# Kernel optimization log

Measured on AMD Instinct MI355X. Metric: run time of the kernel, lower is better.

Reference implementation:

```python
import jax, jax.numpy as jnp
import numpy as np

B, C, HH, WW, QK = 8, 64, 64, 64, 8


def setup_inputs() -> dict:
    key = jax.random.key(0)
    ks = jax.random.split(key, 22)
    s = 0.05
    def W(k, o, i):
        return jax.random.normal(k, (o, i), jnp.float32) * s
    def bvec(k, o):
        return jax.random.normal(k, (o,), jnp.float32) * s
    return {
        "H_in": jax.random.normal(ks[0], (B, C, HH, WW), jnp.float32),
        "M_prev": jax.random.normal(ks[1], (B, C, HH, WW), jnp.float32),
        "wq": W(ks[2], QK, C), "bq": bvec(ks[3], QK),
        "wkh": W(ks[4], QK, C), "bkh": bvec(ks[5], QK),
        "wvh": W(ks[6], C, C), "bvh": bvec(ks[7], C),
        "wkm": W(ks[8], QK, C), "bkm": bvec(ks[9], QK),
        "wvm": W(ks[10], C, C), "bvm": bvec(ks[11], C),
        "wz": W(ks[12], C, 2 * C), "bz": bvec(ks[13], C),
        "wo": W(ks[14], C, 2 * C), "bo": bvec(ks[15], C),
        "wg": W(ks[16], C, 2 * C), "bg": bvec(ks[17], C),
        "wi": W(ks[18], C, 2 * C), "bi": bvec(ks[19], C),
    }


def _conv1x1(w, b, x):
    # x: [B, Cin, N] -> [B, Cout, N]
    return jnp.einsum("oc,bcn->bon", w, x) + b[None, :, None]


def reference(H_in, M_prev, wq, bq, wkh, bkh, wvh, bvh, wkm, bkm, wvm, bvm,
              wz, bz, wo, bo, wg, bg, wi, bi):
    Bn, Cn, Hn, Wn = H_in.shape
    N = Hn * Wn
    h = H_in.reshape(Bn, Cn, N)   # flatten spatial
    m = M_prev.reshape(Bn, Cn, N)

    Q = _conv1x1(wq, bq, h)       # [B, QK, N]
    Kh = _conv1x1(wkh, bkh, h)
    Vh = _conv1x1(wvh, bvh, h)    # [B, C, N]
    Km = _conv1x1(wkm, bkm, m)
    Vm = _conv1x1(wvm, bvm, m)

    scale = jnp.asarray(np.sqrt(Q.shape[1]), Q.dtype)
    # scores: [B, N, N], softmax over last axis
    Ah = jax.nn.softmax(jnp.einsum("bcn,bcm->bnm", Q, Kh) / scale, axis=-1)
    Am = jax.nn.softmax(jnp.einsum("bcn,bcm->bnm", Q, Km) / scale, axis=-1)
    # Zh = Vh @ Ah^T : [B, C, N]
    Zh = jnp.einsum("bcm,bnm->bcn", Vh, Ah)
    Zm = jnp.einsum("bcm,bnm->bcn", Vm, Am)

    Z = _conv1x1(wz, bz, jnp.concatenate([Zh, Zm], axis=1))  # [B, C, N]
    concat = jnp.concatenate([h, Z], axis=1)                  # [B, 2C, N]
    O_t = jax.nn.sigmoid(_conv1x1(wo, bo, concat))
    G_t = jnp.tanh(_conv1x1(wg, bg, concat))
    I_t = jax.nn.sigmoid(_conv1x1(wi, bi, concat))

    M_t = (1.0 - I_t) * m + I_t * G_t
    H_out = O_t * M_t
    return (H_out.reshape(Bn, Cn, Hn, Wn), M_t.reshape(Bn, Cn, Hn, Wn))
```

## Files before the change

### kernel.cpp

```cpp
#include <hip/hip_runtime.h>

#define BATCH 8
#define CC 64
#define NN 4096
#define SCL 0.51006973f

typedef __attribute__((ext_vector_type(8))) short s16x8;
typedef __attribute__((ext_vector_type(4))) short s16x4;
typedef __attribute__((ext_vector_type(4))) float f32x4;
typedef __attribute__((ext_vector_type(2))) unsigned int uint2v;

__device__ __forceinline__ short f2bf(float f) {
  unsigned u = __builtin_bit_cast(unsigned, f);
  u += 0x7fffu + ((u >> 16) & 1u);
  return (short)(u >> 16);
}
__device__ __forceinline__ float bf2f(short h) {
  unsigned u = ((unsigned)(unsigned short)h) << 16;
  return __builtin_bit_cast(float, u);
}
__device__ __forceinline__ unsigned cvt_pk_bf16(float lo, float hi) {
  unsigned r;
  asm volatile("v_cvt_pk_bf16_f32 %0, %1, %2" : "=v"(r) : "v"(lo), "v"(hi));
  return r;
}

__device__ __forceinline__ int kperm(int kk) {
  int hh = (kk >> 5) & 1, g = (kk >> 3) & 3, c = kk & 7;
  return hh * 32 + (c < 4 ? (g << 2) + c : 16 + ((g ^ 2) << 2) + (c - 4));
}

__global__ void prep_weights_kernel(const float* __restrict__ wz, const float* __restrict__ bz,
                                    const float* __restrict__ wo, const float* __restrict__ bo,
                                    const float* __restrict__ wg, const float* __restrict__ bg,
                                    const float* __restrict__ wi, const float* __restrict__ bi,
                                    const float* __restrict__ wq, const float* __restrict__ bq,
                                    const float* __restrict__ wkh, const float* __restrict__ bkh,
                                    const float* __restrict__ wvh, const float* __restrict__ bvh,
                                    const float* __restrict__ wkm, const float* __restrict__ bkm,
                                    const float* __restrict__ wvm, const float* __restrict__ bvm,
                                    short* __restrict__ Weff, float* __restrict__ beff,
                                    short* __restrict__ Wcat, float* __restrict__ bias) {
  int i = blockIdx.x * 256 + threadIdx.x;
  const float* wjs[3] = {wo, wg, wi};
  const float* bjs[3] = {bo, bg, bi};
  const float gsc[3] = {1.44269504f, 2.88539008f, 1.44269504f};
  if (i < 36864) {
    int j = i / 12288, rem = i % 12288, o = rem / 192, k = rem % 192;
    const float* wj = wjs[j];
    float v;
    if (k < 64) {
      v = wj[o * 128 + k];
    } else {
      v = 0.f;
      #pragma unroll 8
      for (int t = 0; t < 64; ++t) v += wj[o * 128 + 64 + t] * wz[t * 128 + (k - 64)];
    }
    Weff[i] = f2bf(v * gsc[j]);
  } else if (i < 37056) {
    int i2 = i - 36864;
    int j = i2 >> 6, o = i2 & 63;
    const float* wj = wjs[j];
    float v = bjs[j][o];
    #pragma unroll 8
    for (int t = 0; t < 64; ++t) v += wj[o * 128 + 64 + t] * bz[t];
    beff[i2] = v * gsc[j];
  } else if (i < 47296) {
    int i2 = i - 37056;
    int src = i2 / 5120, rem = i2 % 5120, row = rem >> 6, col = rem & 63;
    float v;
    if (src == 0) {
      if (row < 64) v = wvh[row * 64 + col];
      else if (row < 72) v = wq[(row - 64) * 64 + col] * SCL;
      else v = wkh[(row - 72) * 64 + col];
    } else {
      if (row < 64) v = wvm[row * 64 + col];
      else if (row < 72) v = wkm[(row - 64) * 64 + col];
      else v = 0.f;
    }
    Wcat[i2] = f2bf(v);
  } else if (i < 47456) {
    int i3 = i - 47296;
    int src = i3 / 80, row = i3 % 80;
    float v;
    if (src == 0) v = (row < 64) ? bvh[row] : (row < 72 ? bq[row - 64] * SCL : bkh[row - 72]);
    else          v = (row < 64) ? bvm[row] : (row < 72 ? bkm[row - 64] : 0.f);
    bias[i3] = v;
  }
}

__global__ __launch_bounds__(256) void proj_kernel(
    const float* __restrict__ H_in, const float* __restrict__ M_prev,
    const short* __restrict__ Wcat, const float* __restrict__ bias,
    short* __restrict__ Qt, short* __restrict__ Kht, short* __restrict__ Kmt,
    short* __restrict__ Vh, short* __restrict__ Vm) {
  int src = blockIdx.x & 1;
  int n0 = ((blockIdx.x >> 1) & 63) << 6;
  int b = blockIdx.x >> 7;
  int tid = threadIdx.x, w = tid >> 6, l = tid & 63, lg = l >> 4, ll = l & 15;

  const float* __restrict__ X = src ? M_prev : H_in;
  short* __restrict__ Vp = src ? Vm : Vh;

  __shared__ __align__(16) short Xt[64][68];
  __shared__ __align__(16) short Ot[64][76];

  {
    int c = tid & 63, q = tid >> 6;
    const float* xs = X + ((size_t)((b << 6) + c)) * NN + n0 + q * 16;
    #pragma unroll
    for (int j = 0; j < 4; ++j) {
      float4 v = *(const float4*)(xs + j * 4);
      Xt[q * 16 + j * 4 + 0][c] = f2bf(v.x);
      Xt[q * 16 + j * 4 + 1][c] = f2bf(v.y);
      Xt[q * 16 + j * 4 + 2][c] = f2bf(v.z);
      Xt[q * 16 + j * 4 + 3][c] = f2bf(v.w);
    }
  }
  __syncthreads();

  f32x4 acc[5];
  #pragma unroll
  for (int ot = 0; ot < 5; ++ot)
    #pragma unroll
    for (int r = 0; r < 4; ++r) acc[ot][r] = bias[src * 80 + ot * 16 + lg * 4 + r];

  #pragma unroll
  for (int kk = 0; kk < 2; ++kk) {
    s16x8 bx = *(const s16x8*)&Xt[w * 16 + ll][kk * 32 + lg * 8];
    #pragma unroll
    for (int ot = 0; ot < 5; ++ot) {
      s16x8 aw = *(const s16x8*)(Wcat + ((size_t)(src * 80 + ot * 16 + ll)) * 64 + kk * 32 + lg * 8);
      acc[ot] = __builtin_amdgcn_mfma_f32_16x16x32_bf16(aw, bx, acc[ot], 0, 0, 0);
    }
  }

  #pragma unroll
  for (int ot = 0; ot < 4; ++ot)
    #pragma unroll
    for (int r = 0; r < 4; ++r)
      Ot[ot * 16 + lg * 4 + r][w * 16 + ll] = f2bf(acc[ot][r]);

  {
    int n = n0 + w * 16 + ll;
    int pr = (n & ~63) + kperm(n & 63);
    #pragma unroll
    for (int r = 0; r < 4; ++r) {
      float v = acc[4][r];
      if (src == 0) {
        if (lg < 2) Qt[((size_t)(b * NN + n)) * 8 + (lg * 4 + r)] = f2bf(v);
        else        Kht[((size_t)(b * NN + pr)) * 8 + ((lg - 2) * 4 + r)] = f2bf(v);
      } else {
        if (lg < 2) Kmt[((size_t)(b * NN + pr)) * 8 + (lg * 4 + r)] = f2bf(v);
      }
    }
  }
  __syncthreads();

  #pragma unroll
  for (int h = 0; h < 2; ++h) {
    int ci = tid + h * 256;
    int row = ci >> 3, seg = ci & 7;
    *(s16x8*)(Vp + ((size_t)((b << 6) + row)) * NN + n0 + seg * 8) =
        *(const s16x8*)&Ot[row][seg * 8];
  }
}

__global__ __launch_bounds__(256, 8) void attn_kernel(
    const short* __restrict__ Qt, const short* __restrict__ Kht, const short* __restrict__ Kmt,
    const short* __restrict__ Vh, const short* __restrict__ Vm,
    short* __restrict__ Zp, float* __restrict__ dnb) {
  unsigned vb = (blockIdx.x & 7) * 256 + (blockIdx.x >> 3);
  int kh = vb >> 10;
  int b  = (vb >> 7) & 7;
  int s  = (vb >> 6) & 1;
  int q0 = (vb & 63) << 6;
  int tid = threadIdx.x;
  int w = tid >> 6, l = tid & 63, lg = l >> 4, ll = l & 15;
  const bool lo32 = (l < 32);

  const short* __restrict__ Kp = s ? Kmt : Kht;
  const short* __restrict__ Vp = s ? Vm : Vh;

  __shared__ __align__(16) short Vt[2][64][64];
  __shared__ __align__(16) short Ktl[2][64][8];
  short* VtF = &Vt[0][0][0];
  short* KtF = &Ktl[0][0][0];

  s16x8 bq = {};
  if (lg == 0) bq = *(const s16x8*)(Qt + ((size_t)(b * NN + q0 + w * 16 + ll)) * 8);
  s16x8 ones;
  #pragma unroll
  for (int i = 0; i < 8; ++i) ones[i] = (short)0x3F80;

  f32x4 accZ[4];
  f32x4 accDn = {0.f, 0.f, 0.f, 0.f};
  #pragma unroll
  for (int cs = 0; cs < 4; ++cs) accZ[cs] = (f32x4){0.f, 0.f, 0.f, 0.f};

  const int vOff0 = ll * 64 + ((lg ^ (ll & 7)) << 3);
  const int vOff1 = ll * 64 + (((lg ^ 4) ^ (ll & 7)) << 3);
  const int kOff  = ll * 8;

  const int row0 = w * 8 + (l >> 3);
  const int swz  = ((l & 7) ^ (l >> 3)) << 3;
  const short* vsrc0 = Vp + ((size_t)((b << 6) + row0)) * NN + kh * 2048 + swz;
  const short* vsrc1 = Vp + ((size_t)((b << 6) + 32 + row0)) * NN + kh * 2048 + swz;
  const short* ksrc  = Kp + ((size_t)(b * NN) + kh * 2048 + l) * 8;

#define GLDS(src_, dst_) \
  __builtin_amdgcn_global_load_lds((const __attribute__((address_space(1))) void*)(src_), \
                                   (__attribute__((address_space(3))) void*)(dst_), 16, 0, 0)
#define STAGE(bufL, ktL) do { \
    GLDS(vsrc0 + (ktL) * 64, VtF + (bufL) * 4096 + w * 512); \
    GLDS(vsrc1 + (ktL) * 64, VtF + (bufL) * 4096 + 2048 + w * 512); \
    if (w == 0) GLDS(ksrc + (ktL) * 512, KtF + (bufL) * 512); \
  } while (0)

  auto compute = [&](int bufL) {
    float p[4][4];
    #pragma unroll
    for (int hh = 0; hh < 2; ++hh) {
      #pragma unroll
      for (int par = 0; par < 2; ++par) {
        s16x8 ak = *(const s16x8*)(KtF + bufL * 512 + (hh * 32 + par * 16) * 8 + kOff);
        f32x4 sc = __builtin_amdgcn_mfma_f32_16x16x32_bf16(ak, bq, (f32x4){0.f,0.f,0.f,0.f}, 0, 0, 0);
        #pragma unroll
        for (int r = 0; r < 4; ++r) p[hh * 2 + par][r] = __builtin_amdgcn_exp2f(sc[r]);
      }
    }
    unsigned wkv[4][2];
    #pragma unroll
    for (int ks = 0; ks < 4; ++ks) {
      wkv[ks][0] = cvt_pk_bf16(p[ks][0], p[ks][1]);
      wkv[ks][1] = cvt_pk_bf16(p[ks][2], p[ks][3]);
    }
    #pragma unroll
    for (int hh = 0; hh < 2; ++hh) {
      unsigned o0 = wkv[hh * 2 + 1][0], o1 = wkv[hh * 2 + 1][1];
      uint2v pr0 = __builtin_amdgcn_permlane32_swap(o0, o0, false, false);
      uint2v pr1 = __builtin_amdgcn_permlane32_swap(o1, o1, false, false);
      unsigned sw0 = lo32 ? pr0.y : pr0.x;
      unsigned sw1 = lo32 ? pr1.y : pr1.x;
      union { unsigned u[4]; s16x8 v; } bpu;
      bpu.u[0] = wkv[hh * 2][0];
      bpu.u[1] = wkv[hh * 2][1];
      bpu.u[2] = sw0;
      bpu.u[3] = sw1;
      s16x8 bp = bpu.v;
      accDn = __builtin_amdgcn_mfma_f32_16x16x32_bf16(ones, bp, accDn, 0, 0, 0);
      const int vo = hh ? vOff1 : vOff0;
      #pragma unroll
      for (int cs = 0; cs < 4; ++cs) {
        s16x8 av = *(const s16x8*)(VtF + bufL * 4096 + cs * 1024 + vo);
        accZ[cs] = __builtin_amdgcn_mfma_f32_16x16x32_bf16(av, bp, accZ[cs], 0, 0, 0);
      }
    }
  };

  STAGE(0, 0);
  #pragma unroll 1
  for (int kt2 = 0; kt2 < 16; ++kt2) {
    int kt = kt2 * 2;
    asm volatile("s_waitcnt vmcnt(0)" ::: "memory");
    __builtin_amdgcn_s_barrier();
    STAGE(1, kt + 1);
    compute(0);
    asm volatile("s_waitcnt vmcnt(0)" ::: "memory");
    __builtin_amdgcn_s_barrier();
    if (kt2 < 15) STAGE(0, kt + 2);
    compute(1);
  }

  #pragma unroll
  for (int cs = 0; cs < 4; ++cs) {
    s16x4 o4;
    #pragma unroll
    for (int r = 0; r < 4; ++r) o4[r] = f2bf(accZ[cs][r]);
    *(s16x4*)(Zp + ((size_t)((kh * 8 + b) * NN + q0 + w * 16 + ll)) * 128 + s * 64 + cs * 16 + lg * 4) = o4;
  }
  if (l < 16)
    dnb[((size_t)(kh * 16 + b * 2 + s)) * NN + q0 + w * 16 + l] = accDn[0];
#undef STAGE
#undef GLDS
}

__global__ __launch_bounds__(256) void gates_kernel(
    const float* __restrict__ H_in, const float* __restrict__ M_prev,
    const short* __restrict__ Zp, const float* __restrict__ dnb,
    const short* __restrict__ Weff, const float* __restrict__ beff,
    float* __restrict__ out) {
  int b = blockIdx.x >> 7;
  int n0 = (blockIdx.x & 127) << 5;
  int tid = threadIdx.x, w = tid >> 6, l = tid & 63, lg = l >> 4, ll = l & 15;
  __shared__ __align__(16) short Xt[32][200];

  {
    int c = tid & 63, q = tid >> 6;
    const float* xs = H_in + ((size_t)((b << 6) + c)) * NN + n0 + q * 8;
    #pragma unroll
    for (int j = 0; j < 2; ++j) {
      float4 v = *(const float4*)(xs + j * 4);
      Xt[q * 8 + j * 4 + 0][c] = f2bf(v.x);
      Xt[q * 8 + j * 4 + 1][c] = f2bf(v.y);
      Xt[q * 8 + j * 4 + 2][c] = f2bf(v.z);
      Xt[q * 8 + j * 4 + 3][c] = f2bf(v.w);
    }
  }
  {
    int n = tid >> 3, cq = tid & 7, sidx = cq >> 2;
    const short* z0 = Zp + ((size_t)(b * NN + n0 + n)) * 128 + cq * 16;
    const short* z1 = Zp + ((size_t)((8 + b) * NN + n0 + n)) * 128 + cq * 16;
    float d0 = dnb[((size_t)(b * 2 + sidx)) * NN + n0 + n];
    float d1 = dnb[((size_t)(16 + b * 2 + sidx)) * NN + n0 + n];
    float rd = __builtin_amdgcn_rcpf(d0 + d1);
    s16x8 a0 = *(const s16x8*)z0;
    s16x8 a1 = *(const s16x8*)z1;
    s16x8 b0 = *(const s16x8*)(z0 + 8);
    s16x8 b1 = *(const s16x8*)(z1 + 8);
    s16x8 o0, o1;
    #pragma unroll
    for (int j = 0; j < 8; ++j) {
      o0[j] = f2bf((bf2f(a0[j]) + bf2f(a1[j])) * rd);
      o1[j] = f2bf((bf2f(b0[j]) + bf2f(b1[j])) * rd);
    }
    *(s16x8*)&Xt[n][64 + cq * 16] = o0;
    *(s16x8*)&Xt[n][64 + cq * 16 + 8] = o1;
  }
  __syncthreads();

  f32x4 acc[3][2];
  #pragma unroll
  for (int j = 0; j < 3; ++j)
    #pragma unroll
    for (int ns = 0; ns < 2; ++ns)
      #pragma unroll
      for (int r = 0; r < 4; ++r) acc[j][ns][r] = beff[j * 64 + w * 16 + lg * 4 + r];

  #pragma unroll
  for (int kk = 0; kk < 6; ++kk) {
    s16x8 aw[3];
    #pragma unroll
    for (int j = 0; j < 3; ++j)
      aw[j] = *(const s16x8*)(Weff + ((size_t)(j * 64 + w * 16 + ll)) * 192 + kk * 32 + lg * 8);
    #pragma unroll
    for (int ns = 0; ns < 2; ++ns) {
      s16x8 bx = *(const s16x8*)&Xt[ns * 16 + ll][kk * 32 + lg * 8];
      #pragma unroll
      for (int j = 0; j < 3; ++j)
        acc[j][ns] = __builtin_amdgcn_mfma_f32_16x16x32_bf16(aw[j], bx, acc[j][ns], 0, 0, 0);
    }
  }

  float* Hout = out;
  float* Mout = out + (size_t)BATCH * CC * NN;
  #pragma unroll
  for (int ns = 0; ns < 2; ++ns) {
    #pragma unroll
    for (int r = 0; r < 4; ++r) {
      int c = w * 16 + lg * 4 + r;
      int n = n0 + ns * 16 + ll;
      size_t idx = ((size_t)((b << 6) + c)) * NN + n;
      float xo = acc[0][ns][r], xg = acc[1][ns][r], xi = acc[2][ns][r];
      float o  = __builtin_amdgcn_rcpf(1.f + __builtin_amdgcn_exp2f(-xo));
      float g  = 2.f * __builtin_amdgcn_rcpf(1.f + __builtin_amdgcn_exp2f(-xg)) - 1.f;
      float ii = __builtin_amdgcn_rcpf(1.f + __builtin_amdgcn_exp2f(-xi));
      float m  = M_prev[idx];
      float mt = (1.f - ii) * m + ii * g;
      Mout[idx] = mt;
      Hout[idx] = o * mt;
    }
  }
}

extern "C" void kernel_launch(void* const* d_in, const int* in_sizes, int n_in,
                              void* d_out, int out_size, void* d_ws, size_t ws_size,
                              hipStream_t stream) {
  (void)in_sizes; (void)n_in; (void)out_size; (void)ws_size;
  const float* H_in  = (const float*)d_in[0];
  const float* M_prev= (const float*)d_in[1];
  const float* wq  = (const float*)d_in[2];
  const float* bq  = (const float*)d_in[3];
  const float* wkh = (const float*)d_in[4];
  const float* bkh = (const float*)d_in[5];
  const float* wvh = (const float*)d_in[6];
  const float* bvh = (const float*)d_in[7];
  const float* wkm = (const float*)d_in[8];
  const float* bkm = (const float*)d_in[9];
  const float* wvm = (const float*)d_in[10];
  const float* bvm = (const float*)d_in[11];
  const float* wz  = (const float*)d_in[12];
  const float* bz  = (const float*)d_in[13];
  const float* wo  = (const float*)d_in[14];
  const float* bo  = (const float*)d_in[15];
  const float* wg  = (const float*)d_in[16];
  const float* bg  = (const float*)d_in[17];
  const float* wi  = (const float*)d_in[18];
  const float* bi  = (const float*)d_in[19];

  char* ws = (char*)d_ws;
  size_t off = 0;
  auto alloc = [&](size_t bytes) -> void* {
    void* p = ws + off;
    off += (bytes + 255) & ~(size_t)255;
    return p;
  };
  short* Weff = (short*)alloc(3 * 64 * 192 * 2);
  float* beff = (float*)alloc(192 * 4);
  short* Wcat = (short*)alloc(2 * 80 * 64 * 2);
  float* bias = (float*)alloc(160 * 4);
  short* Qt   = (short*)alloc((size_t)BATCH * NN * 8 * 2);
  short* Kht  = (short*)alloc((size_t)BATCH * NN * 8 * 2);
  short* Kmt  = (short*)alloc((size_t)BATCH * NN * 8 * 2);
  short* Vh   = (short*)alloc((size_t)BATCH * CC * NN * 2);
  short* Vm   = (short*)alloc((size_t)BATCH * CC * NN * 2);
  short* Zp   = (short*)alloc((size_t)2 * BATCH * NN * 128 * 2);
  float* dnb  = (float*)alloc((size_t)2 * BATCH * 2 * NN * 4);

  prep_weights_kernel<<<186, 256, 0, stream>>>(wz, bz, wo, bo, wg, bg, wi, bi,
                                               wq, bq, wkh, bkh, wvh, bvh, wkm, bkm, wvm, bvm,
                                               Weff, beff, Wcat, bias);
  proj_kernel<<<1024, 256, 0, stream>>>(H_in, M_prev, Wcat, bias, Qt, Kht, Kmt, Vh, Vm);
  attn_kernel<<<2048, 256, 0, stream>>>(Qt, Kht, Kmt, Vh, Vm, Zp, dnb);
  gates_kernel<<<1024, 256, 0, stream>>>(H_in, M_prev, Zp, dnb, Weff, beff, (float*)d_out);
}
```

Before: 191.4 us.

## Process two query tiles per wave in attention to reuse K/V LDS loads

Each attention block now covers 128 queries instead of 64. Each wave computes two 16-query sub-tiles, so every K and V fragment read from LDS feeds two MFMAs, and the grid is halved. This cuts LDS traffic and global K/V staging per query. It also wraps the MFMA section in s_setprio to favour matrix issue. The cost is roughly doubled accumulator registers, with occupancy lowered to 4 blocks, and fewer blocks to hide load latency.

```diff
diff --git a/kernel.cpp b/kernel.cpp
--- a/kernel.cpp
+++ b/kernel.cpp
@@ -166,15 +166,16 @@
   }
 }
 
-__global__ __launch_bounds__(256, 8) void attn_kernel(
+__global__ __launch_bounds__(256, 4) void attn_kernel(
     const short* __restrict__ Qt, const short* __restrict__ Kht, const short* __restrict__ Kmt,
     const short* __restrict__ Vh, const short* __restrict__ Vm,
     short* __restrict__ Zp, float* __restrict__ dnb) {
-  unsigned vb = (blockIdx.x & 7) * 256 + (blockIdx.x >> 3);
-  int kh = vb >> 10;
-  int b  = (vb >> 7) & 7;
-  int s  = (vb >> 6) & 1;
-  int q0 = (vb & 63) << 6;
+  unsigned vb = (blockIdx.x & 7) * 128 + (blockIdx.x >> 3);
+  int qt = vb & 31;
+  int s  = (vb >> 5) & 1;
+  int b  = (vb >> 6) & 7;
+  int kh = (vb >> 9) & 1;
+  int q0 = qt << 7;
   int tid = threadIdx.x;
   int w = tid >> 6, l = tid & 63, lg = l >> 4, ll = l & 15;
   const bool lo32 = (l < 32);
@@ -187,16 +188,20 @@
   short* VtF = &Vt[0][0][0];
   short* KtF = &Ktl[0][0][0];
 
-  s16x8 bq = {};
-  if (lg == 0) bq = *(const s16x8*)(Qt + ((size_t)(b * NN + q0 + w * 16 + ll)) * 8);
+  s16x8 bqA = {}, bqB = {};
+  if (lg == 0) {
+    bqA = *(const s16x8*)(Qt + ((size_t)(b * NN + q0 + w * 32 + ll)) * 8);
+    bqB = *(const s16x8*)(Qt + ((size_t)(b * NN + q0 + w * 32 + 16 + ll)) * 8);
+  }
   s16x8 ones;
   #pragma unroll
   for (int i = 0; i < 8; ++i) ones[i] = (short)0x3F80;
-
-  f32x4 accZ[4];
-  f32x4 accDn = {0.f, 0.f, 0.f, 0.f};
-  #pragma unroll
-  for (int cs = 0; cs < 4; ++cs) accZ[cs] = (f32x4){0.f, 0.f, 0.f, 0.f};
+  const f32x4 fz = {0.f, 0.f, 0.f, 0.f};
+
+  f32x4 accZA[4], accZB[4];
+  f32x4 accDnA = fz, accDnB = fz;
+  #pragma unroll
+  for (int cs = 0; cs < 4; ++cs) { accZA[cs] = fz; accZB[cs] = fz; }
 
   const int vOff0 = ll * 64 + ((lg ^ (ll & 7)) << 3);
   const int vOff1 = ll * 64 + (((lg ^ 4) ^ (ll & 7)) << 3);
@@ -218,43 +223,51 @@
   } while (0)
 
   auto compute = [&](int bufL) {
-    float p[4][4];
     #pragma unroll
     for (int hh = 0; hh < 2; ++hh) {
+      float pA[2][4], pB[2][4];
       #pragma unroll
       for (int par = 0; par < 2; ++par) {
         s16x8 ak = *(const s16x8*)(KtF + bufL * 512 + (hh * 32 + par * 16) * 8 + kOff);
-        f32x4 sc = __builtin_amdgcn_mfma_f32_16x16x32_bf16(ak, bq, (f32x4){0.f,0.f,0.f,0.f}, 0, 0, 0);
+        f32x4 scA = __builtin_amdgcn_mfma_f32_16x16x32_bf16(ak, bqA, fz, 0, 0, 0);
+        f32x4 scB = __builtin_amdgcn_mfma_f32_16x16x32_bf16(ak, bqB, fz, 0, 0, 0);
         #pragma unroll
-        for (int r = 0; r < 4; ++r) p[hh * 2 + par][r] = __builtin_amdgcn_exp2f(sc[r]);
+        for (int r = 0; r < 4; ++r) {
+          pA[par][r] = __builtin_amdgcn_exp2f(scA[r]);
+          pB[par][r] = __builtin_amdgcn_exp2f(scB[r]);
+        }
       }
-    }
-    unsigned wkv[4][2];
-    #pragma unroll
-    for (int ks = 0; ks < 4; ++ks) {
-      wkv[ks][0] = cvt_pk_bf16(p[ks][0], p[ks][1]);
-      wkv[ks][1] = cvt_pk_bf16(p[ks][2], p[ks][3]);
-    }
-    #pragma unroll
-    for (int hh = 0; hh < 2; ++hh) {
-      unsigned o0 = wkv[hh * 2 + 1][0], o1 = wkv[hh * 2 + 1][1];
-      uint2v pr0 = __builtin_amdgcn_permlane32_swap(o0, o0, false, false);
-      uint2v pr1 = __builtin_amdgcn_permlane32_swap(o1, o1, false, false);
-      unsigned sw0 = lo32 ? pr0.y : pr0.x;
-      unsigned sw1 = lo32 ? pr1.y : pr1.x;
-      union { unsigned u[4]; s16x8 v; } bpu;
-      bpu.u[0] = wkv[hh * 2][0];
-      bpu.u[1] = wkv[hh * 2][1];
-      bpu.u[2] = sw0;
-      bpu.u[3] = sw1;
-      s16x8 bp = bpu.v;
-      accDn = __builtin_amdgcn_mfma_f32_16x16x32_bf16(ones, bp, accDn, 0, 0, 0);
+      unsigned a0 = cvt_pk_bf16(pA[0][0], pA[0][1]);
+      unsigned a1 = cvt_pk_bf16(pA[0][2], pA[0][3]);
+      unsigned a2 = cvt_pk_bf16(pA[1][0], pA[1][1]);
+      unsigned a3 = cvt_pk_bf16(pA[1][2], pA[1][3]);
+      unsigned b0 = cvt_pk_bf16(pB[0][0], pB[0][1]);
+      unsigned b1 = cvt_pk_bf16(pB[0][2], pB[0][3]);
+      unsigned b2 = cvt_pk_bf16(pB[1][0], pB[1][1]);
+      unsigned b3 = cvt_pk_bf16(pB[1][2], pB[1][3]);
+      uint2v prA0 = __builtin_amdgcn_permlane32_swap(a2, a2, false, false);
+      uint2v prA1 = __builtin_amdgcn_permlane32_swap(a3, a3, false, false);
+      uint2v prB0 = __builtin_amdgcn_permlane32_swap(b2, b2, false, false);
+      uint2v prB1 = __builtin_amdgcn_permlane32_swap(b3, b3, false, false);
+      union { unsigned u[4]; s16x8 v; } bpA, bpB;
+      bpA.u[0] = a0; bpA.u[1] = a1;
+      bpA.u[2] = lo32 ? prA0.y : prA0.x;
+      bpA.u[3] = lo32 ? prA1.y : prA1.x;
+      bpB.u[0] = b0; bpB.u[1] = b1;
+      bpB.u[2] = lo32 ? prB0.y : prB0.x;
+      bpB.u[3] = lo32 ? prB1.y : prB1.x;
+
       const int vo = hh ? vOff1 : vOff0;
+      __builtin_amdgcn_s_setprio(1);
+      accDnA = __builtin_amdgcn_mfma_f32_16x16x32_bf16(ones, bpA.v, accDnA, 0, 0, 0);
+      accDnB = __builtin_amdgcn_mfma_f32_16x16x32_bf16(ones, bpB.v, accDnB, 0, 0, 0);
       #pragma unroll
       for (int cs = 0; cs < 4; ++cs) {
         s16x8 av = *(const s16x8*)(VtF + bufL * 4096 + cs * 1024 + vo);
-        accZ[cs] = __builtin_amdgcn_mfma_f32_16x16x32_bf16(av, bp, accZ[cs], 0, 0, 0);
+        accZA[cs] = __builtin_amdgcn_mfma_f32_16x16x32_bf16(av, bpA.v, accZA[cs], 0, 0, 0);
+        accZB[cs] = __builtin_amdgcn_mfma_f32_16x16x32_bf16(av, bpB.v, accZB[cs], 0, 0, 0);
       }
+      __builtin_amdgcn_s_setprio(0);
     }
   };
 
@@ -272,15 +285,19 @@
     compute(1);
   }
 
+  int qA = q0 + w * 32 + ll;
   #pragma unroll
   for (int cs = 0; cs < 4; ++cs) {
-    s16x4 o4;
-    #pragma unroll
-    for (int r = 0; r < 4; ++r) o4[r] = f2bf(accZ[cs][r]);
-    *(s16x4*)(Zp + ((size_t)((kh * 8 + b) * NN + q0 + w * 16 + ll)) * 128 + s * 64 + cs * 16 + lg * 4) = o4;
-  }
-  if (l < 16)
-    dnb[((size_t)(kh * 16 + b * 2 + s)) * NN + q0 + w * 16 + l] = accDn[0];
+    s16x4 oA, oB;
+    #pragma unroll
+    for (int r = 0; r < 4; ++r) { oA[r] = f2bf(accZA[cs][r]); oB[r] = f2bf(accZB[cs][r]); }
+    *(s16x4*)(Zp + ((size_t)((kh * 8 + b) * NN + qA)) * 128 + s * 64 + cs * 16 + lg * 4) = oA;
+    *(s16x4*)(Zp + ((size_t)((kh * 8 + b) * NN + qA + 16)) * 128 + s * 64 + cs * 16 + lg * 4) = oB;
+  }
+  if (l < 16) {
+    dnb[((size_t)(kh * 16 + b * 2 + s)) * NN + q0 + w * 32 + l] = accDnA[0];
+    dnb[((size_t)(kh * 16 + b * 2 + s)) * NN + q0 + w * 32 + 16 + l] = accDnB[0];
+  }
 #undef STAGE
 #undef GLDS
 }
@@ -421,6 +438,6 @@
                                                wq, bq, wkh, bkh, wvh, bvh, wkm, bkm, wvm, bvm,
                                                Weff, beff, Wcat, bias);
   proj_kernel<<<1024, 256, 0, stream>>>(H_in, M_prev, Wcat, bias, Qt, Kht, Kmt, Vh, Vm);
-  attn_kernel<<<2048, 256, 0, stream>>>(Qt, Kht, Kmt, Vh, Vm, Zp, dnb);
+  attn_kernel<<<1024, 256, 0, stream>>>(Qt, Kht, Kmt, Vh, Vm, Zp, dnb);
   gates_kernel<<<1024, 256, 0, stream>>>(H_in, M_prev, Zp, dnb, Weff, beff, (float*)d_out);
 }
```

Result: faster. 183.8 us (-4.0%).
